# Kernel tuning notes

Hardware: AMD Instinct MI355X
Metric: run time of the kernel (lower is better)

Reference implementation:

```python
import jax, jax.numpy as jnp
import numpy as np
from jax import lax

DM = 64      # d_model
DI = 128     # d_inner = expand * d_model
DS = 16      # d_state
DC = 4       # d_conv
R = 4        # dt_rank = ceil(d_model/16)
H = 4        # num_heads
NL = 3       # num_mamba_stack
B_READS = 128
L_READ = 512
N_SEQ = 96


def setup_inputs() -> dict:
    key = jax.random.key(0)
    ks = jax.random.split(key, 20)
    f = lambda k, shape, s=0.05: jax.random.normal(k, shape, jnp.float32) * s
    A_init = jnp.broadcast_to(jnp.arange(1, DS + 1, dtype=jnp.float32), (NL, DI, DS))
    return {
        "reads": jax.random.normal(ks[0], (B_READS, L_READ, 4), jnp.float32),
        "sequenced_reads_indices": jax.random.randint(ks[1], (N_SEQ,), 0, B_READS),
        "expander_w": f(ks[2], (DM, 4), 0.3),
        "expander_b": f(ks[3], (DM,)),
        "in_proj_w": f(ks[4], (NL, 2 * DI, DM), 0.1),
        "conv_w": f(ks[5], (NL, DI, 1, DC), 0.3),
        "conv_b": f(ks[6], (NL, DI)),
        "x_proj_w": f(ks[7], (NL, R + 2 * DS, DI), 0.1),
        "dt_w": f(ks[8], (NL, DI, R), 0.3),
        "dt_b": f(ks[9], (NL, DI)),
        "A_log": jnp.log(A_init),
        "D": jnp.ones((NL, DI), jnp.float32),
        "out_w": f(ks[10], (NL, DM, DI), 0.1),
        "ln_w": jnp.ones((NL, DM), jnp.float32),
        "ln_b": jnp.zeros((NL, DM), jnp.float32),
        "query_w": f(ks[11], (DM, 2 * DM), 0.1),
        "query_b": f(ks[12], (DM,)),
        "key_w": f(ks[13], (DM, 2 * DM), 0.1),
        "key_b": f(ks[14], (DM,)),
        "mix_w": f(ks[15], (H, H), 0.3),
        "mix_b": f(ks[16], (H,)),
    }


def _mamba_block(u, in_w, cw, cb, xw, dtw, dtb, A_log, Dp, ow):
    # u: [b, l, DM]
    b, l, _ = u.shape
    xz = u @ in_w.T                              # [b, l, 2*DI]
    x, z = xz[..., :DI], xz[..., DI:]
    # causal depthwise conv along the sequence axis
    xc = lax.conv_general_dilated(
        x.transpose(0, 2, 1), cw, (1,), [(DC - 1, 0)],
        dimension_numbers=("NCH", "OIH", "NCH"), feature_group_count=DI)
    x = jax.nn.silu((xc + cb[None, :, None]).transpose(0, 2, 1))  # [b, l, DI]
    xd = x @ xw.T                                # [b, l, R + 2*DS]
    dt = jax.nn.softplus(xd[..., :R] @ dtw.T + dtb)              # [b, l, DI]
    Bm, Cm = xd[..., R:R + DS], xd[..., R + DS:]                 # [b, l, DS]
    A = -jnp.exp(A_log)                          # [DI, DS]

    def step(h, inp):
        x_t, dt_t, B_t, C_t = inp                # [b,DI],[b,DI],[b,DS],[b,DS]
        h = jnp.exp(dt_t[:, :, None] * A) * h + (dt_t * x_t)[:, :, None] * B_t[:, None, :]
        return h, jnp.einsum("bdn,bn->bd", h, C_t)

    h0 = jnp.zeros((b, DI, DS), u.dtype)
    _, ys = lax.scan(step, h0, (x.swapaxes(0, 1), dt.swapaxes(0, 1),
                                Bm.swapaxes(0, 1), Cm.swapaxes(0, 1)))
    y = ys.swapaxes(0, 1) + x * Dp               # [b, l, DI]
    y = y * jax.nn.silu(z)
    return y @ ow.T                              # [b, l, DM]


def _layer_norm(x, w, b, eps=1e-5):
    m = x.mean(-1, keepdims=True)
    v = ((x - m) ** 2).mean(-1, keepdims=True)
    return (x - m) / jnp.sqrt(v + eps) * w + b


def reference(reads, sequenced_reads_indices, expander_w, expander_b,
              in_proj_w, conv_w, conv_b, x_proj_w, dt_w, dt_b, A_log, D,
              out_w, ln_w, ln_b, query_w, query_b, key_w, key_b, mix_w, mix_b):
    h = reads @ expander_w.T + expander_b        # [b, l, DM]
    for i in range(NL):
        h = _mamba_block(h, in_proj_w[i], conv_w[i], conv_b[i], x_proj_w[i],
                         dt_w[i], dt_b[i], A_log[i], D[i], out_w[i])
        h = jax.nn.relu(_layer_norm(h, ln_w[i], ln_b[i]))
    mean_p = h.mean(1)                           # [b, DM]
    last_p = h[:, -1, :]                         # [b, DM]  (max_pooled in source is dead code)
    enc = jnp.concatenate([mean_p, last_p], axis=-1)   # [b, 2*DM]
    seq = enc[sequenced_reads_indices]                  # [q, 2*DM]
    q = (seq @ query_w.T + query_b).reshape(-1, H, DM // H).transpose(1, 0, 2)
    k = (enc @ key_w.T + key_b).reshape(-1, H, DM // H).transpose(1, 0, 2)
    scores = jnp.einsum("hqd,hkd->qkh", q, k)    # [q, b, H]
    scores = jax.nn.relu(scores) @ mix_w.T + mix_b
    return scores.max(-1)                        # [q, b]
```

## Files before the change

### kernel.cpp

```cpp
#include <hip/hip_runtime.h>
#include <hip/hip_bf16.h>
#include <math.h>

#define NLAYER 3
#define LREADx 512
#define NSEQx  96

typedef _Float16 f16x8 __attribute__((ext_vector_type(8)));
typedef float    f32x4 __attribute__((ext_vector_type(4)));

__device__ __forceinline__ float fsigmoid(float v){ return 1.f/(1.f+__expf(-v)); }
__device__ __forceinline__ float fsoftplus(float v){ return fmaxf(v,0.f) + __logf(1.f + __expf(-fabsf(v))); }

__device__ __forceinline__ unsigned short f2h(float f){
  _Float16 h = (_Float16)f;
  return *reinterpret_cast<unsigned short*>(&h);
}

template<int CTRL>
__device__ __forceinline__ float dpp_add(float v){
  int x = __builtin_amdgcn_update_dpp(0, __float_as_int(v), CTRL, 0xF, 0xF, true);
  return v + __int_as_float(x);
}

__global__ __launch_bounds__(256) void k_exp(const float* __restrict__ reads,
    const float* __restrict__ ew, const float* __restrict__ eb, float* __restrict__ h){
  int idx = blockIdx.x*256 + threadIdx.x;
  int d = idx & 63;
  int row = idx >> 6;
  float4 r4 = *(const float4*)(reads + (size_t)row*4);
  float4 w4 = *(const float4*)(ew + d*4);
  h[idx] = fmaf(r4.x,w4.x, fmaf(r4.y,w4.y, fmaf(r4.z,w4.z, fmaf(r4.w,w4.w, eb[d]))));
}

__global__ __launch_bounds__(256) void k_wcvt(const float* __restrict__ inw,
    const float* __restrict__ ow, const float* __restrict__ xw,
    unsigned short* __restrict__ whf, unsigned short* __restrict__ owh,
    unsigned short* __restrict__ xwh){
  int i = blockIdx.x*256 + threadIdx.x;
  if (i < 49152){ whf[i] = f2h(inw[i]); return; }
  i -= 49152;
  if (i < 24576){ owh[i] = f2h(ow[i]); return; }
  i -= 24576;
  if (i < 18432){
    int l = i / 6144, rem = i % 6144;
    int r = rem >> 7, c = rem & 127;
    xwh[i] = (r < 36) ? f2h(xw[(l*36 + r)*128 + c]) : (unsigned short)0;
  }
}

__global__ __launch_bounds__(256) void k_xzc(const float* __restrict__ h,
    const unsigned short* __restrict__ wb, const float* __restrict__ cw,
    const float* __restrict__ cb, float* __restrict__ x, float* __restrict__ zsil){
  __shared__ float hs_[48][68];
  __shared__ float xp[35][128];
  int t = threadIdx.x;
  int row0 = blockIdx.x*32;
  int l0 = row0 & 511;
  for (int i=t; i<768; i+=256){
    int r = i >> 4, q = i & 15;
    float4 v = make_float4(0.f,0.f,0.f,0.f);
    if (!(l0==0 && r<16)) v = *(const float4*)(h + (size_t)(row0-16+r)*64 + q*4);
    *(float4*)&hs_[r][q*4] = v;
  }
  __syncthreads();
  int w  = __builtin_amdgcn_readfirstlane(t >> 6);
  int ln = t & 63;
  int lr = ln & 15;
  int lk = (ln >> 4)*8;
  f16x8 bf[4][2];
  #pragma unroll
  for (int ct=0; ct<4; ct++)
    #pragma unroll
    for (int ks=0; ks<2; ks++)
      bf[ct][ks] = *(const f16x8*)(wb + (size_t)(w*64 + ct*16 + lr)*64 + ks*32 + lk);
  f16x8 af[3][2];
  #pragma unroll
  for (int m=0; m<3; m++)
    #pragma unroll
    for (int ks=0; ks<2; ks++){
      float4 f0 = *(const float4*)&hs_[m*16+lr][ks*32 + lk];
      float4 f1 = *(const float4*)&hs_[m*16+lr][ks*32 + lk + 4];
      f16x8 a;
      a[0]=(_Float16)f0.x; a[1]=(_Float16)f0.y; a[2]=(_Float16)f0.z; a[3]=(_Float16)f0.w;
      a[4]=(_Float16)f1.x; a[5]=(_Float16)f1.y; a[6]=(_Float16)f1.z; a[7]=(_Float16)f1.w;
      af[m][ks] = a;
    }
  f32x4 acc[3][4];
  #pragma unroll
  for (int m=0;m<3;m++)
    #pragma unroll
    for (int ct=0;ct<4;ct++) acc[m][ct] = (f32x4){0.f,0.f,0.f,0.f};
  #pragma unroll
  for (int ks=0; ks<2; ks++)
    #pragma unroll
    for (int m=0; m<3; m++)
      #pragma unroll
      for (int ct=0; ct<4; ct++)
        acc[m][ct] = __builtin_amdgcn_mfma_f32_16x16x32_f16(af[m][ks], bf[ct][ks], acc[m][ct], 0, 0, 0);
  int colb = w*64;
  #pragma unroll
  for (int m=0; m<3; m++)
    #pragma unroll
    for (int ct=0; ct<4; ct++){
      int col = colb + ct*16 + lr;
      #pragma unroll
      for (int rg=0; rg<4; rg++){
        int rl = m*16 + (ln>>4)*4 + rg;
        float v = acc[m][ct][rg];
        if (col < 128){
          if (rl >= 13) xp[rl-13][col] = v;
        } else {
          if (rl >= 16) zsil[(size_t)(row0 + rl - 16)*128 + (col-128)] = v * fsigmoid(v);
        }
      }
    }
  __syncthreads();
  int c = t & 127, half = t >> 7;
  float4 w4 = *(const float4*)(cw + c*4);
  float bv = cb[c];
  #pragma unroll
  for (int r=half*16; r<half*16+16; r++){
    float a = fmaf(xp[r][c],w4.x, fmaf(xp[r+1][c],w4.y, fmaf(xp[r+2][c],w4.z,
              fmaf(xp[r+3][c],w4.w, bv))));
    x[(size_t)(row0+r)*128 + c] = a * fsigmoid(a);
  }
}

__global__ __launch_bounds__(256) void k_xd(const float* __restrict__ x,
    const unsigned short* __restrict__ xwh, const float* __restrict__ dtw,
    const float* __restrict__ dtb, float* __restrict__ dt, float* __restrict__ bc){
  __shared__ float xst[64][132];
  __shared__ float xdl[64][37];
  int t = threadIdx.x;
  int row0 = blockIdx.x*64;
  for (int i=t; i<2048; i+=256){
    int r = i >> 5, q = i & 31;
    *(float4*)&xst[r][q*4] = *(const float4*)(x + (size_t)(row0+r)*128 + q*4);
  }
  __syncthreads();
  int w = __builtin_amdgcn_readfirstlane(t >> 6);
  int ln = t & 63, lr = ln & 15, kg = ln >> 4;
  f16x8 af[4];
  #pragma unroll
  for (int ks=0; ks<4; ks++){
    float4 f0 = *(const float4*)&xst[w*16+lr][ks*32 + kg*8];
    float4 f1 = *(const float4*)&xst[w*16+lr][ks*32 + kg*8 + 4];
    f16x8 a;
    a[0]=(_Float16)f0.x; a[1]=(_Float16)f0.y; a[2]=(_Float16)f0.z; a[3]=(_Float16)f0.w;
    a[4]=(_Float16)f1.x; a[5]=(_Float16)f1.y; a[6]=(_Float16)f1.z; a[7]=(_Float16)f1.w;
    af[ks] = a;
  }
  f32x4 acc[3];
  #pragma unroll
  for (int ct=0;ct<3;ct++) acc[ct] = (f32x4){0.f,0.f,0.f,0.f};
  #pragma unroll
  for (int ks=0; ks<4; ks++)
    #pragma unroll
    for (int ct=0; ct<3; ct++){
      f16x8 b = *(const f16x8*)(xwh + (size_t)(ct*16 + lr)*128 + ks*32 + kg*8);
      acc[ct] = __builtin_amdgcn_mfma_f32_16x16x32_f16(af[ks], b, acc[ct], 0, 0, 0);
    }
  #pragma unroll
  for (int ct=0; ct<3; ct++){
    int c = ct*16 + lr;
    if (c < 36){
      #pragma unroll
      for (int rg=0; rg<4; rg++) xdl[w*16 + kg*4 + rg][c] = acc[ct][rg];
    }
  }
  __syncthreads();
  int d = t & 127, half = t >> 7;
  float4 w4 = *(const float4*)(dtw + d*4);
  float bv = dtb[d];
  size_t r0 = (size_t)blockIdx.x*64;
  for (int rr=half; rr<64; rr+=2){
    float v = fmaf(xdl[rr][0],w4.x, fmaf(xdl[rr][1],w4.y, fmaf(xdl[rr][2],w4.z,
              fmaf(xdl[rr][3],w4.w, bv))));
    dt[(r0+rr)*128 + d] = fsoftplus(v);
  }
  for (int i=t; i<2048; i+=256){
    int r = i >> 5, cc = i & 31;
    float vv = (cc & 1) ? xdl[r][20 + (cc>>1)] : xdl[r][4 + (cc>>1)];
    bc[(r0+r)*32 + cc] = vv;
  }
}

__global__ __launch_bounds__(256) void k_scan(const float* __restrict__ dt,
    const float* __restrict__ x, const float* __restrict__ zsil,
    const float* __restrict__ bc, const float* __restrict__ alog,
    const float* __restrict__ Dp, float* __restrict__ y){
  __shared__ float dtxb[2][64*68];
  __shared__ float bcb [2][2048];
  __shared__ float ys  [2][2048];
  int t = threadIdx.x;
  int b  = blockIdx.x & 127;
  int dg = blockIdx.x >> 7;
  int dl = t >> 3;
  int np = t & 7;
  int d  = dg*32 + dl;
  float aL1 = -__expf(alog[d*16 + 2*np])     * 1.44269504f;
  float aL2 = -__expf(alog[d*16 + 2*np + 1]) * 1.44269504f;
  float Dv  = Dp[d];
  float hs1 = 0.f, hs2 = 0.f;
  size_t base  = (size_t)b*512*128 + (size_t)dg*32;
  size_t baseb = (size_t)b*512*32;
  int r  = t >> 3;
  int d0 = (t & 7)*4;
  const float* dtA = dt   + base  + (size_t)r*128 + d0;
  const float* xA  = x    + base  + (size_t)r*128 + d0;
  const float* zA  = zsil + base  + (size_t)r*128 + d0;
  const float* bA  = bc   + baseb + (size_t)r*32  + d0;

  auto stage = [&](int bsel, float4 pd0, float4 pd1, float4 px0, float4 px1,
                   float4 pb0, float4 pb1){
    float4 w0 = make_float4(pd0.x, px0.x, pd0.y, px0.y);
    float4 w1 = make_float4(pd0.z, px0.z, pd0.w, px0.w);
    float4 w2 = make_float4(pd1.x, px1.x, pd1.y, px1.y);
    float4 w3 = make_float4(pd1.z, px1.z, pd1.w, px1.w);
    *(float4*)&dtxb[bsel][r*68 + 2*d0]          = w0;
    *(float4*)&dtxb[bsel][r*68 + 2*d0 + 4]      = w1;
    *(float4*)&dtxb[bsel][(r+32)*68 + 2*d0]     = w2;
    *(float4*)&dtxb[bsel][(r+32)*68 + 2*d0 + 4] = w3;
    *(float4*)&bcb[bsel][r*32 + d0]             = pb0;
    *(float4*)&bcb[bsel][r*32 + 1024 + d0]      = pb1;
  };

  {
    float4 pd0 = *(const float4*)(dtA);
    float4 pd1 = *(const float4*)(dtA + 4096);
    float4 px0 = *(const float4*)(xA);
    float4 px1 = *(const float4*)(xA + 4096);
    float4 pb0 = *(const float4*)(bA);
    float4 pb1 = *(const float4*)(bA + 1024);
    stage(0, pd0, pd1, px0, px1, pb0, pb1);
  }
  asm volatile("s_waitcnt lgkmcnt(0)" ::: "memory");
  __builtin_amdgcn_s_barrier();

  for (int c=0;c<8;c++){
    int buf = c & 1;
    float4 nd0, nd1, nx0, nx1, nb0, nb1;
    if (c < 7){
      nd0 = *(const float4*)(dtA + (c+1)*8192);
      nd1 = *(const float4*)(dtA + (c+1)*8192 + 4096);
      nx0 = *(const float4*)(xA  + (c+1)*8192);
      nx1 = *(const float4*)(xA  + (c+1)*8192 + 4096);
      nb0 = *(const float4*)(bA  + (c+1)*2048);
      nb1 = *(const float4*)(bA  + (c+1)*2048 + 1024);
    }
    float4 z0 = *(const float4*)(zA + c*8192);
    float4 z1 = *(const float4*)(zA + c*8192 + 4096);
    #pragma unroll 8
    for (int l=0;l<64;l++){
      float2 dx  = *(const float2*)&dtxb[buf][l*68 + 2*dl];
      float4 bcv = *(const float4*)&bcb[buf][l*32 + 4*np];
      float e1 = __builtin_amdgcn_exp2f(dx.x * aL1);
      float e2 = __builtin_amdgcn_exp2f(dx.x * aL2);
      float dtx = dx.x * dx.y;
      hs1 = fmaf(e1, hs1, dtx * bcv.x);
      hs2 = fmaf(e2, hs2, dtx * bcv.z);
      float p = fmaf(hs1, bcv.y, hs2 * bcv.w);
      p = dpp_add<0x101>(p);
      p = dpp_add<0x102>(p);
      p = dpp_add<0x104>(p);
      if (np == 0) ys[buf][l*32 + dl] = fmaf(dx.y, Dv, p);
    }
    if (c < 7) stage(buf^1, nd0, nd1, nx0, nx1, nb0, nb1);
    asm volatile("s_waitcnt lgkmcnt(0)" ::: "memory");
    __builtin_amdgcn_s_barrier();
    size_t yb = base + (size_t)c*8192;
    float4 s0 = *(const float4*)&ys[buf][4*t];
    float4 s1 = *(const float4*)&ys[buf][4*t + 1024];
    float4 o0 = make_float4(s0.x*z0.x, s0.y*z0.y, s0.z*z0.z, s0.w*z0.w);
    float4 o1 = make_float4(s1.x*z1.x, s1.y*z1.y, s1.z*z1.z, s1.w*z1.w);
    *(float4*)(y + yb + (size_t)r*128 + d0)        = o0;
    *(float4*)(y + yb + (size_t)(r+32)*128 + d0)   = o1;
  }
}

__global__ __launch_bounds__(256) void k_out(const float* __restrict__ y,
    const unsigned short* __restrict__ owh, const float* __restrict__ lnw,
    const float* __restrict__ lnb, float* __restrict__ h){
  __shared__ float yst[64][132];
  int t = threadIdx.x;
  int row0 = blockIdx.x*64;
  for (int i=t; i<2048; i+=256){
    int r = i >> 5, q = i & 31;
    *(float4*)&yst[r][q*4] = *(const float4*)(y + (size_t)(row0+r)*128 + q*4);
  }
  __syncthreads();
  int w = __builtin_amdgcn_readfirstlane(t >> 6);
  int ln = t & 63, lr = ln & 15, kg = ln >> 4;
  f16x8 af[4];
  #pragma unroll
  for (int ks=0; ks<4; ks++){
    float4 f0 = *(const float4*)&yst[w*16+lr][ks*32 + kg*8];
    float4 f1 = *(const float4*)&yst[w*16+lr][ks*32 + kg*8 + 4];
    f16x8 a;
    a[0]=(_Float16)f0.x; a[1]=(_Float16)f0.y; a[2]=(_Float16)f0.z; a[3]=(_Float16)f0.w;
    a[4]=(_Float16)f1.x; a[5]=(_Float16)f1.y; a[6]=(_Float16)f1.z; a[7]=(_Float16)f1.w;
    af[ks] = a;
  }
  f32x4 acc[4];
  #pragma unroll
  for (int ct=0;ct<4;ct++) acc[ct] = (f32x4){0.f,0.f,0.f,0.f};
  #pragma unroll
  for (int ks=0; ks<4; ks++)
    #pragma unroll
    for (int ct=0; ct<4; ct++){
      f16x8 b = *(const f16x8*)(owh + (size_t)(ct*16 + lr)*128 + ks*32 + kg*8);
      acc[ct] = __builtin_amdgcn_mfma_f32_16x16x32_f16(af[ks], b, acc[ct], 0, 0, 0);
    }
  float mean[4], inv[4];
  #pragma unroll
  for (int rg=0; rg<4; rg++){
    float s = acc[0][rg] + acc[1][rg] + acc[2][rg] + acc[3][rg];
    #pragma unroll
    for (int off=1; off<16; off<<=1) s += __shfl_xor(s, off, 64);
    mean[rg] = s * (1.f/64.f);
  }
  #pragma unroll
  for (int rg=0; rg<4; rg++){
    float v = 0.f;
    #pragma unroll
    for (int ct=0; ct<4; ct++){ float dv = acc[ct][rg]-mean[rg]; v += dv*dv; }
    #pragma unroll
    for (int off=1; off<16; off<<=1) v += __shfl_xor(v, off, 64);
    inv[rg] = rsqrtf(v*(1.f/64.f) + 1e-5f);
  }
  float lw[4], lb[4];
  #pragma unroll
  for (int ct=0; ct<4; ct++){ lw[ct] = lnw[ct*16+lr]; lb[ct] = lnb[ct*16+lr]; }
  #pragma unroll
  for (int rg=0; rg<4; rg++){
    int row = row0 + w*16 + kg*4 + rg;
    #pragma unroll
    for (int ct=0; ct<4; ct++){
      float o = (acc[ct][rg]-mean[rg])*inv[rg]*lw[ct] + lb[ct];
      h[(size_t)row*64 + ct*16 + lr] = fmaxf(o, 0.f);
    }
  }
}

__global__ __launch_bounds__(512) void k_pool(const float* __restrict__ h, float* __restrict__ enc){
  __shared__ float ps[8][64];
  int t = threadIdx.x;
  int w = t >> 6, d = t & 63;
  int b = blockIdx.x;
  const float* hb = h + (size_t)b*LREADx*64;
  float s = 0.f;
  #pragma unroll 8
  for (int i=0;i<64;i++) s += hb[(size_t)(w*64+i)*64 + d];
  ps[w][d] = s;
  __syncthreads();
  if (w == 0){
    float acc = 0.f;
    #pragma unroll
    for (int i=0;i<8;i++) acc += ps[i][d];
    enc[b*128 + d]      = acc * (1.f/512.f);
    enc[b*128 + 64 + d] = hb[(size_t)511*64 + d];
  }
}

__global__ __launch_bounds__(256) void k_qk(const float* __restrict__ enc,
    const int* __restrict__ sidx, const float* __restrict__ qw, const float* __restrict__ qb,
    const float* __restrict__ kw, const float* __restrict__ kb,
    float* __restrict__ qbuf, float* __restrict__ kbuf){
  int idx = blockIdx.x*256 + threadIdx.x;
  if (idx < NSEQx*64){
    int qi = idx >> 6, j = idx & 63;
    const float* er = enc + (size_t)sidx[qi]*128;
    const float* wr = qw + j*128;
    float a = qb[j];
    for (int k=0;k<32;k++){
      float4 e4 = *(const float4*)(er + k*4);
      float4 w4 = *(const float4*)(wr + k*4);
      a = fmaf(e4.x,w4.x, fmaf(e4.y,w4.y, fmaf(e4.z,w4.z, fmaf(e4.w,w4.w, a))));
    }
    qbuf[idx] = a;
  } else {
    int i2 = idx - NSEQx*64;
    int ki = i2 >> 6, j = i2 & 63;
    const float* er = enc + (size_t)ki*128;
    const float* wr = kw + j*128;
    float a = kb[j];
    for (int k=0;k<32;k++){
      float4 e4 = *(const float4*)(er + k*4);
      float4 w4 = *(const float4*)(wr + k*4);
      a = fmaf(e4.x,w4.x, fmaf(e4.y,w4.y, fmaf(e4.z,w4.z, fmaf(e4.w,w4.w, a))));
    }
    kbuf[i2] = a;
  }
}

__global__ __launch_bounds__(256) void k_score(const float* __restrict__ qbuf,
    const float* __restrict__ kbuf, const float* __restrict__ mixw,
    const float* __restrict__ mixb, float* __restrict__ out){
  int idx = blockIdx.x*256 + threadIdx.x;
  int ki = idx & 127, qi = idx >> 7;
  const float* qr = qbuf + qi*64;
  const float* kr = kbuf + ki*64;
  float s[4];
  #pragma unroll
  for (int hh=0;hh<4;hh++){
    float a = 0.f;
    #pragma unroll
    for (int k=0;k<4;k++){
      float4 q4 = *(const float4*)(qr + hh*16 + k*4);
      float4 k4 = *(const float4*)(kr + hh*16 + k*4);
      a = fmaf(q4.x,k4.x, fmaf(q4.y,k4.y, fmaf(q4.z,k4.z, fmaf(q4.w,k4.w, a))));
    }
    s[hh] = fmaxf(a, 0.f);
  }
  float best = -1e30f;
  #pragma unroll
  for (int hh=0;hh<4;hh++){
    float v = mixb[hh];
    #pragma unroll
    for (int h2=0;h2<4;h2++) v = fmaf(s[h2], mixw[hh*4+h2], v);
    best = fmaxf(best, v);
  }
  out[idx] = best;
}

extern "C" void kernel_launch(void* const* d_in, const int* in_sizes, int n_in,
                              void* d_out, int out_size, void* d_ws, size_t ws_size,
                              hipStream_t stream) {
  (void)in_sizes; (void)n_in; (void)out_size; (void)ws_size;
  const float* reads = (const float*)d_in[0];
  const int*   sidx  = (const int*)d_in[1];
  const float* ew    = (const float*)d_in[2];
  const float* eb    = (const float*)d_in[3];
  const float* inw   = (const float*)d_in[4];
  const float* cw    = (const float*)d_in[5];
  const float* cb    = (const float*)d_in[6];
  const float* xw    = (const float*)d_in[7];
  const float* dtw   = (const float*)d_in[8];
  const float* dtb   = (const float*)d_in[9];
  const float* alog  = (const float*)d_in[10];
  const float* Dp    = (const float*)d_in[11];
  const float* ow    = (const float*)d_in[12];
  const float* lnw   = (const float*)d_in[13];
  const float* lnb   = (const float*)d_in[14];
  const float* qw    = (const float*)d_in[15];
  const float* qb    = (const float*)d_in[16];
  const float* kw    = (const float*)d_in[17];
  const float* kb    = (const float*)d_in[18];
  const float* mixw  = (const float*)d_in[19];
  const float* mixb  = (const float*)d_in[20];

  float* ws  = (float*)d_ws;
  float* h   = ws;
  float* yx  = ws + 4194304;
  float* zs  = ws + 12582912;
  float* x   = ws + 20971520;
  float* dt  = ws + 29360128;
  float* bc  = ws + 37748736;
  float* enc = ws + 39845888;
  float* qk  = ws + 39862272;
  unsigned short* whf = (unsigned short*)(ws + 39876608);
  unsigned short* owh = whf + 49152;
  unsigned short* xwh = owh + 24576;

  k_wcvt <<<360, 256, 0, stream>>>(inw, ow, xw, whf, owh, xwh);
  k_exp  <<<16384, 256, 0, stream>>>(reads, ew, eb, h);
  for (int l = 0; l < NLAYER; l++){
    k_xzc <<<2048, 256, 0, stream>>>(h, whf + l*16384, cw + l*512, cb + l*128, x, zs);
    k_xd  <<<1024, 256, 0, stream>>>(x, xwh + l*6144, dtw + l*512, dtb + l*128, dt, bc);
    k_scan<<<512, 256, 0, stream>>>(dt, x, zs, bc, alog + l*2048, Dp + l*128, yx);
    k_out <<<1024, 256, 0, stream>>>(yx, owh + l*8192, lnw + l*64, lnb + l*64, h);
  }
  k_pool <<<128, 512, 0, stream>>>(h, enc);
  k_qk   <<<56, 256, 0, stream>>>(enc, sidx, qw, qb, kw, kb, qk, qk + 6144);
  k_score<<<48, 256, 0, stream>>>(qk, qk + 6144, mixw, mixb, (float*)d_out);
}
```

Measured before the change: 430.8 us.

## Store intermediate activations in fp16 and enlarge in-projection row tile

Stores the hidden state, conv output x, gated z, and scan output y in fp16 instead of fp32 in global memory. This halves the traffic for these intermediates and removes the in-kernel fp32-to-fp16 conversions before the MFMA operands. The in-projection/conv kernel also moves from 32 to 64 rows per block, which cuts the redundant 16-row halo recompute per tile. The cost is extra rounding error in the activations passed between layers.

```diff
diff --git a/kernel.cpp b/kernel.cpp
--- a/kernel.cpp
+++ b/kernel.cpp
@@ -7,6 +7,7 @@
 #define NSEQx  96
 
 typedef _Float16 f16x8 __attribute__((ext_vector_type(8)));
+typedef _Float16 f16x4 __attribute__((ext_vector_type(4)));
 typedef float    f32x4 __attribute__((ext_vector_type(4)));
 
 __device__ __forceinline__ float fsigmoid(float v){ return 1.f/(1.f+__expf(-v)); }
@@ -24,13 +25,13 @@
 }
 
 __global__ __launch_bounds__(256) void k_exp(const float* __restrict__ reads,
-    const float* __restrict__ ew, const float* __restrict__ eb, float* __restrict__ h){
+    const float* __restrict__ ew, const float* __restrict__ eb, _Float16* __restrict__ h){
   int idx = blockIdx.x*256 + threadIdx.x;
   int d = idx & 63;
   int row = idx >> 6;
   float4 r4 = *(const float4*)(reads + (size_t)row*4);
   float4 w4 = *(const float4*)(ew + d*4);
-  h[idx] = fmaf(r4.x,w4.x, fmaf(r4.y,w4.y, fmaf(r4.z,w4.z, fmaf(r4.w,w4.w, eb[d]))));
+  h[idx] = (_Float16)fmaf(r4.x,w4.x, fmaf(r4.y,w4.y, fmaf(r4.z,w4.z, fmaf(r4.w,w4.w, eb[d]))));
 }
 
 __global__ __launch_bounds__(256) void k_wcvt(const float* __restrict__ inw,
@@ -49,21 +50,22 @@
   }
 }
 
-__global__ __launch_bounds__(256) void k_xzc(const float* __restrict__ h,
+__global__ __launch_bounds__(256) void k_xzc(const _Float16* __restrict__ h,
     const unsigned short* __restrict__ wb, const float* __restrict__ cw,
-    const float* __restrict__ cb, float* __restrict__ x, float* __restrict__ zsil){
-  __shared__ float hs_[48][68];
-  __shared__ float xp[35][128];
+    const float* __restrict__ cb, _Float16* __restrict__ x, _Float16* __restrict__ zsil){
+  __shared__ _Float16 hs_[80][68];
+  __shared__ _Float16 xp[67][132];
   int t = threadIdx.x;
-  int row0 = blockIdx.x*32;
+  int row0 = blockIdx.x*64;
   int l0 = row0 & 511;
-  for (int i=t; i<768; i+=256){
-    int r = i >> 4, q = i & 15;
-    float4 v = make_float4(0.f,0.f,0.f,0.f);
-    if (!(l0==0 && r<16)) v = *(const float4*)(h + (size_t)(row0-16+r)*64 + q*4);
-    *(float4*)&hs_[r][q*4] = v;
-  }
-  __syncthreads();
+  for (int i=t; i<640; i+=256){
+    int r = i >> 3, q = i & 7;
+    f16x8 v;
+    #pragma unroll
+    for (int e=0;e<8;e++) v[e] = (_Float16)0.f;
+    if (!(l0==0 && r<16)) v = *(const f16x8*)(h + (size_t)(row0-16+r)*64 + q*8);
+    *(f16x8*)&hs_[r][q*8] = v;
+  }
   int w  = __builtin_amdgcn_readfirstlane(t >> 6);
   int ln = t & 63;
   int lr = ln & 15;
@@ -74,33 +76,25 @@
     #pragma unroll
     for (int ks=0; ks<2; ks++)
       bf[ct][ks] = *(const f16x8*)(wb + (size_t)(w*64 + ct*16 + lr)*64 + ks*32 + lk);
-  f16x8 af[3][2];
-  #pragma unroll
-  for (int m=0; m<3; m++)
-    #pragma unroll
-    for (int ks=0; ks<2; ks++){
-      float4 f0 = *(const float4*)&hs_[m*16+lr][ks*32 + lk];
-      float4 f1 = *(const float4*)&hs_[m*16+lr][ks*32 + lk + 4];
-      f16x8 a;
-      a[0]=(_Float16)f0.x; a[1]=(_Float16)f0.y; a[2]=(_Float16)f0.z; a[3]=(_Float16)f0.w;
-      a[4]=(_Float16)f1.x; a[5]=(_Float16)f1.y; a[6]=(_Float16)f1.z; a[7]=(_Float16)f1.w;
-      af[m][ks] = a;
-    }
-  f32x4 acc[3][4];
-  #pragma unroll
-  for (int m=0;m<3;m++)
+  __syncthreads();
+  f32x4 acc[5][4];
+  #pragma unroll
+  for (int m=0;m<5;m++)
     #pragma unroll
     for (int ct=0;ct<4;ct++) acc[m][ct] = (f32x4){0.f,0.f,0.f,0.f};
   #pragma unroll
-  for (int ks=0; ks<2; ks++)
-    #pragma unroll
-    for (int m=0; m<3; m++)
-      #pragma unroll
-      for (int ct=0; ct<4; ct++)
-        acc[m][ct] = __builtin_amdgcn_mfma_f32_16x16x32_f16(af[m][ks], bf[ct][ks], acc[m][ct], 0, 0, 0);
+  for (int m=0; m<5; m++){
+    f16x8 a0 = *(const f16x8*)&hs_[m*16+lr][lk];
+    f16x8 a1 = *(const f16x8*)&hs_[m*16+lr][32 + lk];
+    #pragma unroll
+    for (int ct=0; ct<4; ct++){
+      acc[m][ct] = __builtin_amdgcn_mfma_f32_16x16x32_f16(a0, bf[ct][0], acc[m][ct], 0, 0, 0);
+      acc[m][ct] = __builtin_amdgcn_mfma_f32_16x16x32_f16(a1, bf[ct][1], acc[m][ct], 0, 0, 0);
+    }
+  }
   int colb = w*64;
   #pragma unroll
-  for (int m=0; m<3; m++)
+  for (int m=0; m<5; m++)
     #pragma unroll
     for (int ct=0; ct<4; ct++){
       int col = colb + ct*16 + lr;
@@ -109,9 +103,9 @@
         int rl = m*16 + (ln>>4)*4 + rg;
         float v = acc[m][ct][rg];
         if (col < 128){
-          if (rl >= 13) xp[rl-13][col] = v;
+          if (rl >= 13) xp[rl-13][col] = (_Float16)v;
         } else {
-          if (rl >= 16) zsil[(size_t)(row0 + rl - 16)*128 + (col-128)] = v * fsigmoid(v);
+          if (rl >= 16) zsil[(size_t)(row0 + rl - 16)*128 + (col-128)] = (_Float16)(v * fsigmoid(v));
         }
       }
     }
@@ -120,37 +114,30 @@
   float4 w4 = *(const float4*)(cw + c*4);
   float bv = cb[c];
   #pragma unroll
-  for (int r=half*16; r<half*16+16; r++){
-    float a = fmaf(xp[r][c],w4.x, fmaf(xp[r+1][c],w4.y, fmaf(xp[r+2][c],w4.z,
-              fmaf(xp[r+3][c],w4.w, bv))));
-    x[(size_t)(row0+r)*128 + c] = a * fsigmoid(a);
-  }
-}
-
-__global__ __launch_bounds__(256) void k_xd(const float* __restrict__ x,
+  for (int r=half*32; r<half*32+32; r++){
+    float a = fmaf((float)xp[r][c],w4.x, fmaf((float)xp[r+1][c],w4.y,
+              fmaf((float)xp[r+2][c],w4.z, fmaf((float)xp[r+3][c],w4.w, bv))));
+    x[(size_t)(row0+r)*128 + c] = (_Float16)(a * fsigmoid(a));
+  }
+}
+
+__global__ __launch_bounds__(256) void k_xd(const _Float16* __restrict__ x,
     const unsigned short* __restrict__ xwh, const float* __restrict__ dtw,
     const float* __restrict__ dtb, float* __restrict__ dt, float* __restrict__ bc){
-  __shared__ float xst[64][132];
+  __shared__ _Float16 xst[64][136];
   __shared__ float xdl[64][37];
   int t = threadIdx.x;
   int row0 = blockIdx.x*64;
-  for (int i=t; i<2048; i+=256){
-    int r = i >> 5, q = i & 31;
-    *(float4*)&xst[r][q*4] = *(const float4*)(x + (size_t)(row0+r)*128 + q*4);
+  for (int i=t; i<1024; i+=256){
+    int r = i >> 4, q = i & 15;
+    *(f16x8*)&xst[r][q*8] = *(const f16x8*)(x + (size_t)(row0+r)*128 + q*8);
   }
   __syncthreads();
   int w = __builtin_amdgcn_readfirstlane(t >> 6);
   int ln = t & 63, lr = ln & 15, kg = ln >> 4;
   f16x8 af[4];
   #pragma unroll
-  for (int ks=0; ks<4; ks++){
-    float4 f0 = *(const float4*)&xst[w*16+lr][ks*32 + kg*8];
-    float4 f1 = *(const float4*)&xst[w*16+lr][ks*32 + kg*8 + 4];
-    f16x8 a;
-    a[0]=(_Float16)f0.x; a[1]=(_Float16)f0.y; a[2]=(_Float16)f0.z; a[3]=(_Float16)f0.w;
-    a[4]=(_Float16)f1.x; a[5]=(_Float16)f1.y; a[6]=(_Float16)f1.z; a[7]=(_Float16)f1.w;
-    af[ks] = a;
-  }
+  for (int ks=0; ks<4; ks++) af[ks] = *(const f16x8*)&xst[w*16+lr][ks*32 + kg*8];
   f32x4 acc[3];
   #pragma unroll
   for (int ct=0;ct<3;ct++) acc[ct] = (f32x4){0.f,0.f,0.f,0.f};
@@ -187,9 +174,9 @@
 }
 
 __global__ __launch_bounds__(256) void k_scan(const float* __restrict__ dt,
-    const float* __restrict__ x, const float* __restrict__ zsil,
+    const _Float16* __restrict__ x, const _Float16* __restrict__ zsil,
     const float* __restrict__ bc, const float* __restrict__ alog,
-    const float* __restrict__ Dp, float* __restrict__ y){
+    const float* __restrict__ Dp, _Float16* __restrict__ y){
   __shared__ float dtxb[2][64*68];
   __shared__ float bcb [2][2048];
   __shared__ float ys  [2][2048];
@@ -207,17 +194,17 @@
   size_t baseb = (size_t)b*512*32;
   int r  = t >> 3;
   int d0 = (t & 7)*4;
-  const float* dtA = dt   + base  + (size_t)r*128 + d0;
-  const float* xA  = x    + base  + (size_t)r*128 + d0;
-  const float* zA  = zsil + base  + (size_t)r*128 + d0;
-  const float* bA  = bc   + baseb + (size_t)r*32  + d0;
-
-  auto stage = [&](int bsel, float4 pd0, float4 pd1, float4 px0, float4 px1,
+  const float*    dtA = dt   + base  + (size_t)r*128 + d0;
+  const _Float16* xA  = x    + base  + (size_t)r*128 + d0;
+  const _Float16* zA  = zsil + base  + (size_t)r*128 + d0;
+  const float*    bA  = bc   + baseb + (size_t)r*32  + d0;
+
+  auto stage = [&](int bsel, float4 pd0, float4 pd1, f16x4 px0, f16x4 px1,
                    float4 pb0, float4 pb1){
-    float4 w0 = make_float4(pd0.x, px0.x, pd0.y, px0.y);
-    float4 w1 = make_float4(pd0.z, px0.z, pd0.w, px0.w);
-    float4 w2 = make_float4(pd1.x, px1.x, pd1.y, px1.y);
-    float4 w3 = make_float4(pd1.z, px1.z, pd1.w, px1.w);
+    float4 w0 = make_float4(pd0.x, (float)px0[0], pd0.y, (float)px0[1]);
+    float4 w1 = make_float4(pd0.z, (float)px0[2], pd0.w, (float)px0[3]);
+    float4 w2 = make_float4(pd1.x, (float)px1[0], pd1.y, (float)px1[1]);
+    float4 w3 = make_float4(pd1.z, (float)px1[2], pd1.w, (float)px1[3]);
     *(float4*)&dtxb[bsel][r*68 + 2*d0]          = w0;
     *(float4*)&dtxb[bsel][r*68 + 2*d0 + 4]      = w1;
     *(float4*)&dtxb[bsel][(r+32)*68 + 2*d0]     = w2;
@@ -229,8 +216,8 @@
   {
     float4 pd0 = *(const float4*)(dtA);
     float4 pd1 = *(const float4*)(dtA + 4096);
-    float4 px0 = *(const float4*)(xA);
-    float4 px1 = *(const float4*)(xA + 4096);
+    f16x4  px0 = *(const f16x4*)(xA);
+    f16x4  px1 = *(const f16x4*)(xA + 4096);
     float4 pb0 = *(const float4*)(bA);
     float4 pb1 = *(const float4*)(bA + 1024);
     stage(0, pd0, pd1, px0, px1, pb0, pb1);
@@ -240,17 +227,18 @@
 
   for (int c=0;c<8;c++){
     int buf = c & 1;
-    float4 nd0, nd1, nx0, nx1, nb0, nb1;
+    float4 nd0, nd1, nb0, nb1;
+    f16x4  nx0, nx1;
     if (c < 7){
       nd0 = *(const float4*)(dtA + (c+1)*8192);
       nd1 = *(const float4*)(dtA + (c+1)*8192 + 4096);
-      nx0 = *(const float4*)(xA  + (c+1)*8192);
-      nx1 = *(const float4*)(xA  + (c+1)*8192 + 4096);
+      nx0 = *(const f16x4*)(xA  + (c+1)*8192);
+      nx1 = *(const f16x4*)(xA  + (c+1)*8192 + 4096);
       nb0 = *(const float4*)(bA  + (c+1)*2048);
       nb1 = *(const float4*)(bA  + (c+1)*2048 + 1024);
     }
-    float4 z0 = *(const float4*)(zA + c*8192);
-    float4 z1 = *(const float4*)(zA + c*8192 + 4096);
+    f16x4 z0 = *(const f16x4*)(zA + c*8192);
+    f16x4 z1 = *(const f16x4*)(zA + c*8192 + 4096);
     #pragma unroll 8
     for (int l=0;l<64;l++){
       float2 dx  = *(const float2*)&dtxb[buf][l*68 + 2*dl];
@@ -272,36 +260,32 @@
     size_t yb = base + (size_t)c*8192;
     float4 s0 = *(const float4*)&ys[buf][4*t];
     float4 s1 = *(const float4*)&ys[buf][4*t + 1024];
-    float4 o0 = make_float4(s0.x*z0.x, s0.y*z0.y, s0.z*z0.z, s0.w*z0.w);
-    float4 o1 = make_float4(s1.x*z1.x, s1.y*z1.y, s1.z*z1.z, s1.w*z1.w);
-    *(float4*)(y + yb + (size_t)r*128 + d0)        = o0;
-    *(float4*)(y + yb + (size_t)(r+32)*128 + d0)   = o1;
-  }
-}
-
-__global__ __launch_bounds__(256) void k_out(const float* __restrict__ y,
+    f16x4 o0, o1;
+    o0[0] = (_Float16)(s0.x*(float)z0[0]); o0[1] = (_Float16)(s0.y*(float)z0[1]);
+    o0[2] = (_Float16)(s0.z*(float)z0[2]); o0[3] = (_Float16)(s0.w*(float)z0[3]);
+    o1[0] = (_Float16)(s1.x*(float)z1[0]); o1[1] = (_Float16)(s1.y*(float)z1[1]);
+    o1[2] = (_Float16)(s1.z*(float)z1[2]); o1[3] = (_Float16)(s1.w*(float)z1[3]);
+    *(f16x4*)(y + yb + (size_t)r*128 + d0)      = o0;
+    *(f16x4*)(y + yb + (size_t)(r+32)*128 + d0) = o1;
+  }
+}
+
+__global__ __launch_bounds__(256) void k_out(const _Float16* __restrict__ y,
     const unsigned short* __restrict__ owh, const float* __restrict__ lnw,
-    const float* __restrict__ lnb, float* __restrict__ h){
-  __shared__ float yst[64][132];
+    const float* __restrict__ lnb, _Float16* __restrict__ h){
+  __shared__ _Float16 yst[64][136];
   int t = threadIdx.x;
   int row0 = blockIdx.x*64;
-  for (int i=t; i<2048; i+=256){
-    int r = i >> 5, q = i & 31;
-    *(float4*)&yst[r][q*4] = *(const float4*)(y + (size_t)(row0+r)*128 + q*4);
+  for (int i=t; i<1024; i+=256){
+    int r = i >> 4, q = i & 15;
+    *(f16x8*)&yst[r][q*8] = *(const f16x8*)(y + (size_t)(row0+r)*128 + q*8);
   }
   __syncthreads();
   int w = __builtin_amdgcn_readfirstlane(t >> 6);
   int ln = t & 63, lr = ln & 15, kg = ln >> 4;
   f16x8 af[4];
   #pragma unroll
-  for (int ks=0; ks<4; ks++){
-    float4 f0 = *(const float4*)&yst[w*16+lr][ks*32 + kg*8];
-    float4 f1 = *(const float4*)&yst[w*16+lr][ks*32 + kg*8 + 4];
-    f16x8 a;
-    a[0]=(_Float16)f0.x; a[1]=(_Float16)f0.y; a[2]=(_Float16)f0.z; a[3]=(_Float16)f0.w;
-    a[4]=(_Float16)f1.x; a[5]=(_Float16)f1.y; a[6]=(_Float16)f1.z; a[7]=(_Float16)f1.w;
-    af[ks] = a;
-  }
+  for (int ks=0; ks<4; ks++) af[ks] = *(const f16x8*)&yst[w*16+lr][ks*32 + kg*8];
   f32x4 acc[4];
   #pragma unroll
   for (int ct=0;ct<4;ct++) acc[ct] = (f32x4){0.f,0.f,0.f,0.f};
@@ -338,20 +322,20 @@
     #pragma unroll
     for (int ct=0; ct<4; ct++){
       float o = (acc[ct][rg]-mean[rg])*inv[rg]*lw[ct] + lb[ct];
-      h[(size_t)row*64 + ct*16 + lr] = fmaxf(o, 0.f);
-    }
-  }
-}
-
-__global__ __launch_bounds__(512) void k_pool(const float* __restrict__ h, float* __restrict__ enc){
+      h[(size_t)row*64 + ct*16 + lr] = (_Float16)fmaxf(o, 0.f);
+    }
+  }
+}
+
+__global__ __launch_bounds__(512) void k_pool(const _Float16* __restrict__ h, float* __restrict__ enc){
   __shared__ float ps[8][64];
   int t = threadIdx.x;
   int w = t >> 6, d = t & 63;
   int b = blockIdx.x;
-  const float* hb = h + (size_t)b*LREADx*64;
+  const _Float16* hb = h + (size_t)b*LREADx*64;
   float s = 0.f;
   #pragma unroll 8
-  for (int i=0;i<64;i++) s += hb[(size_t)(w*64+i)*64 + d];
+  for (int i=0;i<64;i++) s += (float)hb[(size_t)(w*64+i)*64 + d];
   ps[w][d] = s;
   __syncthreads();
   if (w == 0){
@@ -359,7 +343,7 @@
     #pragma unroll
     for (int i=0;i<8;i++) acc += ps[i][d];
     enc[b*128 + d]      = acc * (1.f/512.f);
-    enc[b*128 + 64 + d] = hb[(size_t)511*64 + d];
+    enc[b*128 + 64 + d] = (float)hb[(size_t)511*64 + d];
   }
 }
 
@@ -451,10 +435,10 @@
   const float* mixb  = (const float*)d_in[20];
 
   float* ws  = (float*)d_ws;
-  float* h   = ws;
-  float* yx  = ws + 4194304;
-  float* zs  = ws + 12582912;
-  float* x   = ws + 20971520;
+  _Float16* h  = (_Float16*)(ws);
+  _Float16* yx = (_Float16*)(ws + 4194304);
+  _Float16* zs = (_Float16*)(ws + 12582912);
+  _Float16* x  = (_Float16*)(ws + 20971520);
   float* dt  = ws + 29360128;
   float* bc  = ws + 37748736;
   float* enc = ws + 39845888;
@@ -466,7 +450,7 @@
   k_wcvt <<<360, 256, 0, stream>>>(inw, ow, xw, whf, owh, xwh);
   k_exp  <<<16384, 256, 0, stream>>>(reads, ew, eb, h);
   for (int l = 0; l < NLAYER; l++){
-    k_xzc <<<2048, 256, 0, stream>>>(h, whf + l*16384, cw + l*512, cb + l*128, x, zs);
+    k_xzc <<<1024, 256, 0, stream>>>(h, whf + l*16384, cw + l*512, cb + l*128, x, zs);
     k_xd  <<<1024, 256, 0, stream>>>(x, xwh + l*6144, dtw + l*512, dtb + l*128, dt, bc);
     k_scan<<<512, 256, 0, stream>>>(dt, x, zs, bc, alog + l*2048, Dp + l*128, yx);
     k_out <<<1024, 256, 0, stream>>>(yx, owh + l*8192, lnw + l*64, lnb + l*64, h);
```

Result: faster. 389.0 us (-9.7%).
